# Kernel optimization log

Hardware: AMD Instinct MI355X
Metric: run time of the kernel (lower is better)

## Reference

```python
import jax, jax.numpy as jnp
import numpy as np

B, L, H = 16, 96, 150
WED, PED = 100, 50
EMB = WED + PED  # 150
WV, TV = 50000, 50


def setup_inputs() -> dict:
    key = jax.random.key(0)
    ks = jax.random.split(key, 16)
    f = lambda k, shape, s=0.1: jax.random.normal(k, shape, dtype=jnp.float32) * s
    return {
        "words_idx_tensor": jax.random.randint(ks[0], (B, L), 0, WV),
        "pos_idx_tensor": jax.random.randint(ks[1], (B, L), 0, TV),
        "max_length": L,
        "word_emb": f(ks[2], (WV, WED)),
        "tag_emb": f(ks[3], (TV, PED)),
        "W_ih0": f(ks[4], (2, 4 * H, EMB)),        # layer 0, both dirs
        "W_ih_rest": f(ks[5], (3, 2, 4 * H, 2 * H)),  # layers 1-3
        "W_hh": f(ks[6], (4, 2, 4 * H, H)),
        "b_ih": f(ks[7], (4, 2, 4 * H)),
        "b_hh": f(ks[8], (4, 2, 4 * H)),
        "w1": jax.random.uniform(ks[9], (1,), jnp.float32, -1.0, 1.0),
        "w2": jax.random.uniform(ks[10], (1,), jnp.float32, -1.0, 1.0),
        "w3": jax.random.uniform(ks[11], (1,), jnp.float32, -1.0, 1.0),
        "w4": jax.random.uniform(ks[12], (1,), jnp.float32, -1.0, 1.0),
        "mlp_w1": f(ks[13], (100, 4 * H)),
        "mlp_b1": jnp.zeros((100,), jnp.float32),
        "mlp_w2": f(ks[14], (1, 100)),
        "mlp_b2": jnp.zeros((1,), jnp.float32),
    }


def _lstm_dir(x, Wih, Whh, bi, bh):
    # x: [B, T, D] -> hidden states [B, T, H]; torch LSTM cell math (gate order i,f,g,o)
    Bx = x.shape[0]
    Hh = Whh.shape[-1]
    pre = jnp.einsum('btd,gd->btg', x, Wih) + bi + bh  # input contribution, [B,T,4H]

    def step(carry, p):
        h, c = carry
        gates = p + h @ Whh.T
        i, fg, g, o = jnp.split(gates, 4, axis=-1)
        i, fg, o = jax.nn.sigmoid(i), jax.nn.sigmoid(fg), jax.nn.sigmoid(o)
        g = jnp.tanh(g)
        c = fg * c + i * g
        h = o * jnp.tanh(c)
        return (h, c), h

    init = (jnp.zeros((Bx, Hh), x.dtype), jnp.zeros((Bx, Hh), x.dtype))
    _, hs = jax.lax.scan(step, init, pre.transpose(1, 0, 2))  # [T,B,H]
    return hs.transpose(1, 0, 2)


def _bilstm(x, W_ih0, W_ih_rest, W_hh, b_ih, b_hh):
    inp = x
    for layer in range(4):  # fixed structural loop over layers
        outs = []
        for d in range(2):  # forward / backward direction
            Wih = W_ih0[d] if layer == 0 else W_ih_rest[layer - 1, d]
            xs = inp if d == 0 else inp[:, ::-1]
            hs = _lstm_dir(xs, Wih, W_hh[layer, d], b_ih[layer, d], b_hh[layer, d])
            outs.append(hs if d == 0 else hs[:, ::-1])
        inp = jnp.concatenate(outs, axis=-1)  # [B,T,2H]
    return inp


def reference(words_idx_tensor, pos_idx_tensor, max_length, word_emb, tag_emb,
              W_ih0, W_ih_rest, W_hh, b_ih, b_hh, w1, w2, w3, w4,
              mlp_w1, mlp_b1, mlp_w2, mlp_b2):
    we = word_emb[words_idx_tensor[:, :max_length]]   # [B,L,WED]
    te = tag_emb[pos_idx_tensor[:, :max_length]]      # [B,L,PED]
    embeds = jnp.concatenate([we, te], axis=-1)       # [B,L,EMB]
    out = _bilstm(embeds, W_ih0, W_ih_rest, W_hh, b_ih, b_hh)  # [B,L,2H]
    Bn, Lm, C = out.shape
    # features[l1, b, l2] = cat(out[b, l1], out[b, l2])  -> [L, B, L, 4H]
    ht = out.transpose(1, 0, 2)  # [L,B,2H]
    head = jnp.broadcast_to(ht[:, :, None, :], (Lm, Bn, Lm, C))
    dep = jnp.broadcast_to(out[None, :, :, :], (Lm, Bn, Lm, C))
    features = jnp.concatenate([head, dep], axis=-1)  # [L,B,L,4H]
    # w1*f + w2*f^2 + w3*f^3 + w4*f^4 via Horner (single fused elementwise pass)
    poly = features * (w1[0] + features * (w2[0] + features * (w3[0] + features * w4[0])))
    h1 = jnp.tanh(poly @ mlp_w1.T + mlp_b1)           # [L,B,L,100]
    edge_scores = h1 @ mlp_w2.T + mlp_b2              # [L,B,L,1]
    return edge_scores
```

## Files before the change

kernel.cpp:

```cpp
#include <hip/hip_runtime.h>

typedef __attribute__((ext_vector_type(8))) _Float16 half8;
typedef __attribute__((ext_vector_type(4))) _Float16 half4;
typedef __attribute__((ext_vector_type(4))) float float4v;

__device__ __forceinline__ float4v mfma16h(half8 a, half8 b, float4v c) {
  return __builtin_amdgcn_mfma_f32_16x16x32_f16(a, b, c, 0, 0, 0);
}

__device__ __forceinline__ half8 cat44h(half4 a, half4 b) {
  half8 r;
  r[0]=a[0]; r[1]=a[1]; r[2]=a[2]; r[3]=a[3];
  r[4]=b[0]; r[5]=b[1]; r[6]=b[2]; r[7]=b[3];
  return r;
}

__device__ __forceinline__ void split_f16(float x, _Float16& hi, _Float16& lo) {
  hi = (_Float16)x;
  lo = (_Float16)(x - (float)hi);
}

#define KLOG2E 1.442695041f
__device__ __forceinline__ float fast_tanh(float x) {
  float z = __builtin_amdgcn_exp2f(2.f * KLOG2E * x);
  return 1.f - 2.f * __builtin_amdgcn_rcpf(1.f + z);
}


__global__ void prep_kernel(
    const float* __restrict__ Wih0,
    const float* __restrict__ WihR,
    const float* __restrict__ Whh,
    const float* __restrict__ bih,
    const float* __restrict__ bhh,
    const float* __restrict__ w1m,
    const float* __restrict__ b1v,
    _Float16* __restrict__ whh_f,
    _Float16* __restrict__ wih_f,
    _Float16* __restrict__ wpr_f,
    float* __restrict__ bsum, float* __restrict__ b1cat)
{
  const int N_whh  = 8 * 40 * 5 * 512;
  const int N_wih0 = 2 * 40 * 5 * 512;
  const int N_wihr = 6 * 40 * 10 * 512;
  const int N_wpr  = 16 * 10 * 512;
  const int N_bs   = 8 * 640;
  const int total  = N_whh + N_wih0 + N_wihr + N_wpr + N_bs + 256;
  for (int i = blockIdx.x * blockDim.x + threadIdx.x; i < total;
       i += gridDim.x * blockDim.x) {
    int idx = i;
    if (idx < N_whh) {
      int e = idx & 7, lane = (idx >> 3) & 63, r = idx >> 9;
      int kc = r % 5; r /= 5; int nt = r % 40; int ld = r / 40;
      int jrow = (nt >> 2) * 16 + (lane & 15);
      int g = (nt & 3) * 150 + jrow;
      int k = 32 * kc + 16 * (e >> 2) + 4 * (lane >> 4) + (e & 3);
      float v = (jrow < 150 && k < 150) ? Whh[((size_t)ld * 600 + g) * 150 + k] : 0.f;
      v *= ((nt & 3) == 2) ? (2.f * KLOG2E) : (-KLOG2E);
      whh_f[idx] = (_Float16)v;
      continue;
    }
    idx -= N_whh;
    if (idx < N_wih0) {
      int e = idx & 7, lane = (idx >> 3) & 63, r = idx >> 9;
      int kc = r % 5; r /= 5; int nt = r % 40; int dir = r / 40;
      int jrow = (nt >> 2) * 16 + (lane & 15);
      int g = (nt & 3) * 150 + jrow;
      int k = 32 * kc + 16 * (e >> 2) + 4 * (lane >> 4) + (e & 3);
      float v = (jrow < 150 && k < 150) ? Wih0[((size_t)dir * 600 + g) * 150 + k] : 0.f;
      v *= ((nt & 3) == 2) ? (2.f * KLOG2E) : (-KLOG2E);
      wih_f[idx] = (_Float16)v;
      continue;
    }
    idx -= N_wih0;
    if (idx < N_wihr) {
      int e = idx & 7, lane = (idx >> 3) & 63, r = idx >> 9;
      int kc = r % 10; r /= 10; int nt = r % 40; int ld = r / 40;
      int jrow = (nt >> 2) * 16 + (lane & 15);
      int g = (nt & 3) * 150 + jrow;
      int k = 32 * kc + 16 * (e >> 2) + 4 * (lane >> 4) + (e & 3);
      float v = (jrow < 150 && k < 300) ? WihR[((size_t)ld * 600 + g) * 300 + k] : 0.f;
      v *= ((nt & 3) == 2) ? (2.f * KLOG2E) : (-KLOG2E);
      wih_f[N_wih0 + idx] = (_Float16)v;
      continue;
    }
    idx -= N_wihr;
    if (idx < N_wpr) {
      int e = idx & 7, lane = (idx >> 3) & 63, r = idx >> 9;
      int kc = r % 10; int nt = r / 10;
      int ko = 16 * nt + (lane & 15);
      int k = 32 * kc + 16 * (e >> 2) + 4 * (lane >> 4) + (e & 3);
      float v = 0.f;
      if (k < 300) {
        if (ko < 100) v = w1m[(size_t)ko * 600 + k];
        else if (ko < 200) v = w1m[(size_t)(ko - 100) * 600 + 300 + k];
      }
      wpr_f[idx] = (_Float16)v;
      continue;
    }
    idx -= N_wpr;
    if (idx < N_bs) {
      int ld = idx / 640, gp = idx - 640 * ld;
      int nt = gp >> 4, lrow = gp & 15;
      int jrow = (nt >> 2) * 16 + lrow;
      int g = (nt & 3) * 150 + jrow;
      float v = (jrow < 150) ? bih[ld * 600 + g] + bhh[ld * 600 + g] : 0.f;
      v *= ((nt & 3) == 2) ? (2.f * KLOG2E) : (-KLOG2E);
      bsum[idx] = v;
      continue;
    }
    idx -= N_bs;
    b1cat[idx] = (idx < 100) ? b1v[idx] : ((idx < 200) ? b1v[idx - 100] : 0.f);
  }
}

__global__ void embed_kernel(const int* __restrict__ widx, const int* __restrict__ pidx,
    const float* __restrict__ wemb, const float* __restrict__ temb,
    _Float16* __restrict__ xa, _Float16* __restrict__ xb)
{
  int row = blockIdx.x;
  int j = threadIdx.x;
  int b = row & 15, t = row >> 4;
  float v = 0.f;
  if (j < 100) v = wemb[(size_t)widx[b * 96 + t] * 100 + j];
  else if (j < 150) v = temb[(size_t)pidx[b * 96 + t] * 50 + (j - 100)];
  size_t o = (size_t)row * 320 + j;
  xa[o] = (_Float16)v;
  if (j >= 300) xb[o] = (_Float16)0.f;
}

template <int KC>
__global__ __launch_bounds__(512) void pregemm_kernel(
    const _Float16* __restrict__ x_h,
    const _Float16* __restrict__ wih_f,
    const float* __restrict__ bsum_l,
    float* __restrict__ pre)
{
  const int t = blockIdx.x, dir = blockIdx.y;
  const int tid = threadIdx.x, wv = tid >> 6, lane = tid & 63;
  const int lrow = lane & 15, lgrp = lane >> 4;
  const _Float16* wf = wih_f + (size_t)dir * 40 * KC * 512;
  float4v acc[5];
#pragma unroll
  for (int tt = 0; tt < 5; ++tt) acc[tt] = (float4v){0.f, 0.f, 0.f, 0.f};
  const size_t arow = ((size_t)t * 16 + lrow) * 320;
#pragma unroll
  for (int kc = 0; kc < KC; ++kc) {
    int co = 32 * kc + 4 * lgrp;
    half8 ah = cat44h(*(const half4*)(x_h + arow + co),
                      *(const half4*)(x_h + arow + co + 16));
#pragma unroll
    for (int tt = 0; tt < 5; ++tt) {
      int nt = 5 * wv + tt;
      const size_t wo = ((size_t)(nt * KC + kc) * 64 + lane) * 8;
      half8 bw = *(const half8*)(wf + wo);
      acc[tt] = mfma16h(ah, bw, acc[tt]);
    }
  }
  float* po = pre + (size_t)(dir * 96 + t) * 10240;
  const float* bs = bsum_l + dir * 640;
#pragma unroll
  for (int tt = 0; tt < 5; ++tt) {
    int nt = 5 * wv + tt;
    float bv = bs[16 * nt + lrow];
    float4v v;
#pragma unroll
    for (int jj = 0; jj < 4; ++jj) v[jj] = acc[tt][jj] + bv;
    int tid_s = (nt >> 2) * 64 + lgrp * 16 + lrow;
    *(float4v*)(po + (size_t)tid_s * 16 + (nt & 3) * 4) = v;
  }
}

__global__ __launch_bounds__(640, 1) void scan_kernel(
    const float* __restrict__ pre,
    const _Float16* __restrict__ whh_f,
    _Float16* __restrict__ xo,
    int layer)
{
  const int dir = blockIdx.x;
  const int tid = threadIdx.x, wv = tid >> 6, lane = tid & 63;
  const int lrow = lane & 15, lgrp = lane >> 4;

  __shared__ __align__(16) _Float16 hb[2][16 * 172];

  for (int i = tid; i < 2 * 16 * 172; i += 640)
    (&hb[0][0])[i] = (_Float16)0.f;

  const _Float16* b_base = whh_f + (size_t)(layer * 2 + dir) * 40 * 5 * 512;
  half8 Bw[4][5];
#pragma unroll
  for (int tt = 0; tt < 4; ++tt)
#pragma unroll
    for (int kc = 0; kc < 5; ++kc) {
      size_t o = ((size_t)((4 * wv + tt) * 5 + kc) * 64 + lane) * 8;
      Bw[tt][kc] = *(const half8*)(b_base + o);
    }

  float cst[4] = {0.f, 0.f, 0.f, 0.f};
  const int j = 16 * wv + lrow;
  const int kcj = j >> 5, wj = j & 31;
  const int hoff = kcj * 32 + ((wj >> 2) & 3) * 8 + (wj >> 4) * 4 + (wj & 3);
  const bool jok = (j < 150);

  const int t0 = dir ? 95 : 0;
  const long pincv = dir ? -2560 : 2560;
  const long xinc = dir ? -(16 * 320) : (16 * 320);
  const float4v* pc = (const float4v*)pre + ((size_t)(dir * 96 + t0) * 640 + tid) * 4;
  _Float16* xop = xo + ((size_t)t0 * 16 + 4 * lgrp) * 320 + dir * 150 + j;

  float4v pfA[4], pfB[4];
#pragma unroll
  for (int i = 0; i < 4; ++i) pfA[i] = pc[i];
  pc += pincv;
#pragma unroll
  for (int i = 0; i < 4; ++i) pfB[i] = pc[i];
  pc += pincv;
  __syncthreads();

#define SCAN_STEP(PF, HIN, HOUT)                                          \
  {                                                                       \
    _Pragma("unroll")                                                     \
    for (int kc = 0; kc < 5; ++kc) {                                      \
      const int ao = lrow * 172 + kc * 32 + lgrp * 8;                     \
      half8 ah = *(const half8*)((HIN) + ao);                             \
      _Pragma("unroll")                                                   \
      for (int tt = 0; tt < 4; ++tt)                                      \
        PF[tt] = mfma16h(ah, Bw[tt][kc], PF[tt]);                         \
    }                                                                     \
    _Pragma("unroll")                                                     \
    for (int jj = 0; jj < 4; ++jj) {                                      \
      float zi = __builtin_amdgcn_exp2f(PF[0][jj]);                       \
      float zf = __builtin_amdgcn_exp2f(PF[1][jj]);                       \
      float zg = __builtin_amdgcn_exp2f(PF[2][jj]);                       \
      float zo = __builtin_amdgcn_exp2f(PF[3][jj]);                       \
      float rf = __builtin_amdgcn_rcpf(1.f + zf);                         \
      float r2 = __builtin_amdgcn_rcpf((1.f + zi) * (zg + 1.f));          \
      float c = cst[jj] * rf + (zg - 1.f) * r2;                           \
      cst[jj] = c;                                                        \
      float zc = __builtin_amdgcn_exp2f(2.f * KLOG2E * c);                \
      float r3 = __builtin_amdgcn_rcpf((1.f + zo) * (zc + 1.f));          \
      float h = (zc - 1.f) * r3;                                          \
      _Float16 hv = (_Float16)h;                                          \
      (HOUT)[(4 * lgrp + jj) * 172 + hoff] = hv;                          \
      if (jok) xop[jj * 320] = hv;                                        \
    }                                                                     \
    _Pragma("unroll")                                                     \
    for (int i = 0; i < 4; ++i) PF[i] = pc[i];                            \
    pc += pincv;                                                          \
    xop += xinc;                                                          \
    __syncthreads();                                                      \
  }

#pragma unroll 1
  for (int s2 = 0; s2 < 48; ++s2) {
    SCAN_STEP(pfA, hb[0], hb[1]);
    SCAN_STEP(pfB, hb[1], hb[0]);
  }
#undef SCAN_STEP
}

__global__ void poly_kernel(const _Float16* __restrict__ xi,
    _Float16* __restrict__ po_h, _Float16* __restrict__ po_l,
    const float* __restrict__ w1, const float* __restrict__ w2,
    const float* __restrict__ w3, const float* __restrict__ w4)
{
  int i = blockIdx.x * 256 + threadIdx.x;
  if (i >= 1536 * 320) return;
  float x = (float)xi[i];
  float p = x * (w1[0] + x * (w2[0] + x * (w3[0] + x * w4[0])));
  _Float16 h, l; split_f16(p, h, l);
  po_h[i] = h; po_l[i] = l;
}

__global__ __launch_bounds__(512) void proj_kernel(
    const _Float16* __restrict__ p_h, const _Float16* __restrict__ p_l,
    const _Float16* __restrict__ wpr_f,
    const float* __restrict__ b1cat,
    float* __restrict__ AD)
{
  const int t = blockIdx.x;
  const int tid = threadIdx.x, wv = tid >> 6, lane = tid & 63;
  const int lrow = lane & 15, lgrp = lane >> 4;
  float4v acc[2] = {{0.f, 0.f, 0.f, 0.f}, {0.f, 0.f, 0.f, 0.f}};
  const size_t arow = ((size_t)t * 16 + lrow) * 320;
#pragma unroll
  for (int kc = 0; kc < 10; ++kc) {
    int co = 32 * kc + 4 * lgrp;
    half8 ah = cat44h(*(const half4*)(p_h + arow + co),
                      *(const half4*)(p_h + arow + co + 16));
    half8 al = cat44h(*(const half4*)(p_l + arow + co),
                      *(const half4*)(p_l + arow + co + 16));
#pragma unroll
    for (int tt = 0; tt < 2; ++tt) {
      int nt = 2 * wv + tt;
      size_t wo = ((size_t)(nt * 10 + kc) * 64 + lane) * 8;
      half8 bw = *(const half8*)(wpr_f + wo);
      acc[tt] = mfma16h(ah, bw, acc[tt]);
      acc[tt] = mfma16h(al, bw, acc[tt]);
    }
  }
#pragma unroll
  for (int tt = 0; tt < 2; ++tt) {
    int ko = 16 * (2 * wv + tt) + lrow;
    float bv = b1cat[ko];
#pragma unroll
    for (int jj = 0; jj < 4; ++jj)
      AD[((size_t)t * 16 + 4 * lgrp + jj) * 256 + ko] = acc[tt][jj] + bv;
  }
}

__global__ __launch_bounds__(768) void combine_kernel(
    const float* __restrict__ AD, const float* __restrict__ w2v,
    const float* __restrict__ b2v, float* __restrict__ out)
{
  const int bb = blockIdx.x & 15, lt = blockIdx.x >> 4;
  const int tid = threadIdx.x;
  __shared__ float Dl[100 * 97];
  __shared__ float Al[100 * 9];
  __shared__ float w2s[100];
  for (int i = tid; i < 96 * 32; i += 768) {
    int ld = i >> 5, f4 = i & 31;
    if (f4 < 25) {
      float4v v = *(const float4v*)(AD + ((size_t)ld * 16 + bb) * 256 + 100 + 4 * f4);
      int k0 = 4 * f4;
      Dl[(k0 + 0) * 97 + ld] = v[0];
      Dl[(k0 + 1) * 97 + ld] = v[1];
      Dl[(k0 + 2) * 97 + ld] = v[2];
      Dl[(k0 + 3) * 97 + ld] = v[3];
    }
  }
  for (int i = tid; i < 8 * 32; i += 768) {
    int lh = i >> 5, f4 = i & 31;
    if (f4 < 25) {
      int lseq = lt * 8 + lh;
      float4v v = *(const float4v*)(AD + ((size_t)lseq * 16 + bb) * 256 + 4 * f4);
      int k0 = 4 * f4;
      Al[(k0 + 0) * 9 + lh] = v[0];
      Al[(k0 + 1) * 9 + lh] = v[1];
      Al[(k0 + 2) * 9 + lh] = v[2];
      Al[(k0 + 3) * 9 + lh] = v[3];
    }
  }
  if (tid < 100) w2s[tid] = w2v[tid];
  __syncthreads();
  int lh = tid / 96, ld = tid - 96 * lh;
  float s = 0.f;
#pragma unroll 4
  for (int k = 0; k < 100; ++k) {
    float x = Al[k * 9 + lh] + Dl[k * 97 + ld];
    s += w2s[k] * fast_tanh(x);
  }
  out[((size_t)(lt * 8 + lh) * 16 + bb) * 96 + ld] = s + b2v[0];
}

extern "C" void kernel_launch(void* const* d_in, const int* in_sizes, int n_in,
                              void* d_out, int out_size, void* d_ws, size_t ws_size,
                              hipStream_t stream)
{
  const int*   widx = (const int*)d_in[0];
  const int*   pidx = (const int*)d_in[1];
  const float* wemb = (const float*)d_in[3];
  const float* temb = (const float*)d_in[4];
  const float* Wih0 = (const float*)d_in[5];
  const float* WihR = (const float*)d_in[6];
  const float* Whh  = (const float*)d_in[7];
  const float* bih  = (const float*)d_in[8];
  const float* bhh  = (const float*)d_in[9];
  const float* w1   = (const float*)d_in[10];
  const float* w2   = (const float*)d_in[11];
  const float* w3   = (const float*)d_in[12];
  const float* w4   = (const float*)d_in[13];
  const float* w1m  = (const float*)d_in[14];
  const float* b1v  = (const float*)d_in[15];
  const float* w2m  = (const float*)d_in[16];
  const float* b2v  = (const float*)d_in[17];
  float* out = (float*)d_out;

  char* ws = (char*)d_ws;
  size_t off = 0;
  auto alloc = [&](size_t bytes) -> char* {
    char* p = ws + off;
    off = (off + bytes + 255) & ~(size_t)255;
    return p;
  };
  _Float16* WHH_F = (_Float16*)alloc(819200ull * 2);
  _Float16* WIH_F = (_Float16*)alloc(1433600ull * 2);
  _Float16* WPR_F = (_Float16*)alloc(81920ull * 2);
  float* BSUM = (float*)alloc(5120ull * 4);
  float* B1C  = (float*)alloc(256ull * 4);
  _Float16* XA = (_Float16*)alloc(491520ull * 2);
  _Float16* XB = (_Float16*)alloc(491520ull * 2);
  _Float16* PH = (_Float16*)alloc(491520ull * 2);
  _Float16* PL = (_Float16*)alloc(491520ull * 2);
  float* PRE = (float*)alloc(1966080ull * 4);
  float* AD  = (float*)alloc(1536ull * 256 * 4);

  prep_kernel<<<512, 256, 0, stream>>>(Wih0, WihR, Whh, bih, bhh, w1m, b1v,
      WHH_F, WIH_F, WPR_F, BSUM, B1C);
  embed_kernel<<<1536, 320, 0, stream>>>(widx, pidx, wemb, temb, XA, XB);

  for (int layer = 0; layer < 4; ++layer) {
    const _Float16* xin = (layer & 1) ? XB : XA;
    _Float16* xout = (layer & 1) ? XA : XB;
    const float* bsl = BSUM + layer * 2 * 640;
    if (layer == 0) {
      pregemm_kernel<5><<<dim3(96, 2), 512, 0, stream>>>(xin, WIH_F, bsl, PRE);
    } else {
      size_t wo = 204800ull + (size_t)(layer - 1) * 409600ull;
      pregemm_kernel<10><<<dim3(96, 2), 512, 0, stream>>>(xin, WIH_F + wo, bsl, PRE);
    }
    scan_kernel<<<2, 640, 0, stream>>>(PRE, WHH_F, xout, layer);
  }
  poly_kernel<<<1920, 256, 0, stream>>>(XA, PH, PL, w1, w2, w3, w4);
  proj_kernel<<<96, 512, 0, stream>>>(PH, PL, WPR_F, B1C, AD);
  combine_kernel<<<192, 768, 0, stream>>>(AD, w2m, b2v, out);
}
```

Measured before the change: 543.7 us.

## Fuse embed into prep, poly into proj, batch reciprocals and lighten scan barrier

The embedding gather moves into the prep kernel's grid-stride loop, and the polynomial split moves into the projection kernel through shared memory. Together these remove two launches and the PH/PL round trip through global memory. In the sequential scan, the per-element reciprocals are batched pairwise to cut rcp count on the critical path. __syncthreads is replaced by an LDS-only waitcnt plus s_barrier, which avoids waiting on outstanding global stores. The batched reciprocals add multiplies and some overflow risk in the products.

```diff
diff --git a/kernel.cpp b/kernel.cpp
--- a/kernel.cpp
+++ b/kernel.cpp
@@ -35,17 +35,21 @@
     const float* __restrict__ bhh,
     const float* __restrict__ w1m,
     const float* __restrict__ b1v,
+    const int* __restrict__ widx, const int* __restrict__ pidx,
+    const float* __restrict__ wemb, const float* __restrict__ temb,
     _Float16* __restrict__ whh_f,
     _Float16* __restrict__ wih_f,
     _Float16* __restrict__ wpr_f,
-    float* __restrict__ bsum, float* __restrict__ b1cat)
+    float* __restrict__ bsum, float* __restrict__ b1cat,
+    _Float16* __restrict__ xa, _Float16* __restrict__ xb)
 {
   const int N_whh  = 8 * 40 * 5 * 512;
   const int N_wih0 = 2 * 40 * 5 * 512;
   const int N_wihr = 6 * 40 * 10 * 512;
   const int N_wpr  = 16 * 10 * 512;
   const int N_bs   = 8 * 640;
-  const int total  = N_whh + N_wih0 + N_wihr + N_wpr + N_bs + 256;
+  const int N_emb  = 1536 * 320;
+  const int total  = N_whh + N_wih0 + N_wihr + N_wpr + N_bs + 256 + N_emb;
   for (int i = blockIdx.x * blockDim.x + threadIdx.x; i < total;
        i += gridDim.x * blockDim.x) {
     int idx = i;
@@ -110,23 +114,21 @@
       continue;
     }
     idx -= N_bs;
-    b1cat[idx] = (idx < 100) ? b1v[idx] : ((idx < 200) ? b1v[idx - 100] : 0.f);
-  }
-}
-
-__global__ void embed_kernel(const int* __restrict__ widx, const int* __restrict__ pidx,
-    const float* __restrict__ wemb, const float* __restrict__ temb,
-    _Float16* __restrict__ xa, _Float16* __restrict__ xb)
-{
-  int row = blockIdx.x;
-  int j = threadIdx.x;
-  int b = row & 15, t = row >> 4;
-  float v = 0.f;
-  if (j < 100) v = wemb[(size_t)widx[b * 96 + t] * 100 + j];
-  else if (j < 150) v = temb[(size_t)pidx[b * 96 + t] * 50 + (j - 100)];
-  size_t o = (size_t)row * 320 + j;
-  xa[o] = (_Float16)v;
-  if (j >= 300) xb[o] = (_Float16)0.f;
+    if (idx < 256) {
+      b1cat[idx] = (idx < 100) ? b1v[idx] : ((idx < 200) ? b1v[idx - 100] : 0.f);
+      continue;
+    }
+    idx -= 256;
+    {
+      int row = idx / 320, j = idx - 320 * row;
+      int b = row & 15, t = row >> 4;
+      float v = 0.f;
+      if (j < 100) v = wemb[(size_t)widx[b * 96 + t] * 100 + j];
+      else if (j < 150) v = temb[(size_t)pidx[b * 96 + t] * 50 + (j - 100)];
+      xa[idx] = (_Float16)v;
+      if (j >= 300) xb[idx] = (_Float16)0.f;
+    }
+  }
 }
 
 template <int KC>
@@ -227,28 +229,57 @@
       for (int tt = 0; tt < 4; ++tt)                                      \
         PF[tt] = mfma16h(ah, Bw[tt][kc], PF[tt]);                         \
     }                                                                     \
+    float zo_[4], Dq[4], Nq[4], cv[4];                                    \
     _Pragma("unroll")                                                     \
     for (int jj = 0; jj < 4; ++jj) {                                      \
       float zi = __builtin_amdgcn_exp2f(PF[0][jj]);                       \
       float zf = __builtin_amdgcn_exp2f(PF[1][jj]);                       \
       float zg = __builtin_amdgcn_exp2f(PF[2][jj]);                       \
-      float zo = __builtin_amdgcn_exp2f(PF[3][jj]);                       \
-      float rf = __builtin_amdgcn_rcpf(1.f + zf);                         \
-      float r2 = __builtin_amdgcn_rcpf((1.f + zi) * (zg + 1.f));          \
-      float c = cst[jj] * rf + (zg - 1.f) * r2;                           \
-      cst[jj] = c;                                                        \
-      float zc = __builtin_amdgcn_exp2f(2.f * KLOG2E * c);                \
-      float r3 = __builtin_amdgcn_rcpf((1.f + zo) * (zc + 1.f));          \
-      float h = (zc - 1.f) * r3;                                          \
-      _Float16 hv = (_Float16)h;                                          \
-      (HOUT)[(4 * lgrp + jj) * 172 + hoff] = hv;                          \
-      if (jok) xop[jj * 320] = hv;                                        \
+      zo_[jj]  = __builtin_amdgcn_exp2f(PF[3][jj]);                       \
+      float tq = (1.f + zi) * (zg + 1.f);                                 \
+      float fq = 1.f + zf;                                                \
+      Dq[jj] = tq * fq;                                                   \
+      Nq[jj] = cst[jj] * tq + (zg - 1.f) * fq;                            \
+    }                                                                     \
+    {                                                                     \
+      float rP0 = __builtin_amdgcn_rcpf(Dq[0] * Dq[1]);                   \
+      float rP1 = __builtin_amdgcn_rcpf(Dq[2] * Dq[3]);                   \
+      cv[0] = Nq[0] * rP0 * Dq[1];                                        \
+      cv[1] = Nq[1] * rP0 * Dq[0];                                        \
+      cv[2] = Nq[2] * rP1 * Dq[3];                                        \
+      cv[3] = Nq[3] * rP1 * Dq[2];                                        \
+    }                                                                     \
+    float zc_[4], Eq[4];                                                  \
+    _Pragma("unroll")                                                     \
+    for (int jj = 0; jj < 4; ++jj) {                                      \
+      cst[jj] = cv[jj];                                                   \
+      zc_[jj] = __builtin_amdgcn_exp2f(2.f * KLOG2E * cv[jj]);            \
+      Eq[jj] = (1.f + zo_[jj]) * (zc_[jj] + 1.f);                         \
+    }                                                                     \
+    {                                                                     \
+      float rE0 = __builtin_amdgcn_rcpf(Eq[0] * Eq[1]);                   \
+      float rE1 = __builtin_amdgcn_rcpf(Eq[2] * Eq[3]);                   \
+      float hv0 = (zc_[0] - 1.f) * rE0 * Eq[1];                           \
+      float hv1 = (zc_[1] - 1.f) * rE0 * Eq[0];                           \
+      float hv2 = (zc_[2] - 1.f) * rE1 * Eq[3];                           \
+      float hv3 = (zc_[3] - 1.f) * rE1 * Eq[2];                           \
+      _Float16 h0 = (_Float16)hv0, h1 = (_Float16)hv1;                    \
+      _Float16 h2 = (_Float16)hv2, h3 = (_Float16)hv3;                    \
+      (HOUT)[(4 * lgrp + 0) * 172 + hoff] = h0;                           \
+      (HOUT)[(4 * lgrp + 1) * 172 + hoff] = h1;                           \
+      (HOUT)[(4 * lgrp + 2) * 172 + hoff] = h2;                          \
+      (HOUT)[(4 * lgrp + 3) * 172 + hoff] = h3;                           \
+      if (jok) {                                                          \
+        xop[0 * 320] = h0; xop[1 * 320] = h1;                             \
+        xop[2 * 320] = h2; xop[3 * 320] = h3;                             \
+      }                                                                   \
     }                                                                     \
     _Pragma("unroll")                                                     \
     for (int i = 0; i < 4; ++i) PF[i] = pc[i];                            \
     pc += pincv;                                                          \
     xop += xinc;                                                          \
-    __syncthreads();                                                      \
+    asm volatile("s_waitcnt lgkmcnt(0)" ::: "memory");                    \
+    __builtin_amdgcn_s_barrier();                                         \
   }
 
 #pragma unroll 1
@@ -259,37 +290,36 @@
 #undef SCAN_STEP
 }
 
-__global__ void poly_kernel(const _Float16* __restrict__ xi,
-    _Float16* __restrict__ po_h, _Float16* __restrict__ po_l,
-    const float* __restrict__ w1, const float* __restrict__ w2,
-    const float* __restrict__ w3, const float* __restrict__ w4)
-{
-  int i = blockIdx.x * 256 + threadIdx.x;
-  if (i >= 1536 * 320) return;
-  float x = (float)xi[i];
-  float p = x * (w1[0] + x * (w2[0] + x * (w3[0] + x * w4[0])));
-  _Float16 h, l; split_f16(p, h, l);
-  po_h[i] = h; po_l[i] = l;
-}
-
 __global__ __launch_bounds__(512) void proj_kernel(
-    const _Float16* __restrict__ p_h, const _Float16* __restrict__ p_l,
+    const _Float16* __restrict__ xi,
     const _Float16* __restrict__ wpr_f,
     const float* __restrict__ b1cat,
+    const float* __restrict__ w1, const float* __restrict__ w2,
+    const float* __restrict__ w3, const float* __restrict__ w4,
     float* __restrict__ AD)
 {
   const int t = blockIdx.x;
   const int tid = threadIdx.x, wv = tid >> 6, lane = tid & 63;
   const int lrow = lane & 15, lgrp = lane >> 4;
+  __shared__ __align__(16) _Float16 ph[16 * 328];
+  __shared__ __align__(16) _Float16 pl[16 * 328];
+  {
+    float c1 = w1[0], c2 = w2[0], c3 = w3[0], c4 = w4[0];
+    for (int e = tid; e < 16 * 320; e += 512) {
+      int row = e / 320, col = e - 320 * row;
+      float x = (float)xi[(size_t)t * 5120 + e];
+      float p = x * (c1 + x * (c2 + x * (c3 + x * c4)));
+      _Float16 h, l; split_f16(p, h, l);
+      ph[row * 328 + col] = h; pl[row * 328 + col] = l;
+    }
+  }
+  __syncthreads();
   float4v acc[2] = {{0.f, 0.f, 0.f, 0.f}, {0.f, 0.f, 0.f, 0.f}};
-  const size_t arow = ((size_t)t * 16 + lrow) * 320;
 #pragma unroll
   for (int kc = 0; kc < 10; ++kc) {
-    int co = 32 * kc + 4 * lgrp;
-    half8 ah = cat44h(*(const half4*)(p_h + arow + co),
-                      *(const half4*)(p_h + arow + co + 16));
-    half8 al = cat44h(*(const half4*)(p_l + arow + co),
-                      *(const half4*)(p_l + arow + co + 16));
+    int co = lrow * 328 + 32 * kc + 4 * lgrp;
+    half8 ah = cat44h(*(const half4*)(ph + co), *(const half4*)(ph + co + 16));
+    half8 al = cat44h(*(const half4*)(pl + co), *(const half4*)(pl + co + 16));
 #pragma unroll
     for (int tt = 0; tt < 2; ++tt) {
       int nt = 2 * wv + tt;
@@ -390,14 +420,12 @@
   float* B1C  = (float*)alloc(256ull * 4);
   _Float16* XA = (_Float16*)alloc(491520ull * 2);
   _Float16* XB = (_Float16*)alloc(491520ull * 2);
-  _Float16* PH = (_Float16*)alloc(491520ull * 2);
-  _Float16* PL = (_Float16*)alloc(491520ull * 2);
   float* PRE = (float*)alloc(1966080ull * 4);
   float* AD  = (float*)alloc(1536ull * 256 * 4);
 
   prep_kernel<<<512, 256, 0, stream>>>(Wih0, WihR, Whh, bih, bhh, w1m, b1v,
-      WHH_F, WIH_F, WPR_F, BSUM, B1C);
-  embed_kernel<<<1536, 320, 0, stream>>>(widx, pidx, wemb, temb, XA, XB);
+      widx, pidx, wemb, temb,
+      WHH_F, WIH_F, WPR_F, BSUM, B1C, XA, XB);
 
   for (int layer = 0; layer < 4; ++layer) {
     const _Float16* xin = (layer & 1) ? XB : XA;
@@ -411,7 +439,6 @@
     }
     scan_kernel<<<2, 640, 0, stream>>>(PRE, WHH_F, xout, layer);
   }
-  poly_kernel<<<1920, 256, 0, stream>>>(XA, PH, PL, w1, w2, w3, w4);
-  proj_kernel<<<96, 512, 0, stream>>>(PH, PL, WPR_F, B1C, AD);
+  proj_kernel<<<96, 512, 0, stream>>>(XA, WPR_F, B1C, w1, w2, w3, w4, AD);
   combine_kernel<<<192, 768, 0, stream>>>(AD, w2m, b2v, out);
 }
```

Result: faster. 529.2 us (-2.7%).
